# Optimization experiments

Measured on AMD Instinct MI355X. Metric: run time of the kernel, lower is better.

## Reference

```python
import jax, jax.numpy as jnp
import numpy as np

B, T = 128, 512
V, P, K = 10002, 500, 20
DC, DP, DT = 300, 100, 50
D = DC + DP + DT
H = 256


def setup_inputs() -> dict:
    key = jax.random.key(0)
    ks = jax.random.split(key, 21)
    s = lambda i, shape: jax.random.normal(ks[i], shape, jnp.float32) * 0.05
    return dict(
        x=jax.random.randint(ks[0], (B, T), 0, V),
        y=jax.random.randint(ks[1], (B, T), 0, K),
        pre_tags=jax.random.randint(ks[2], (B, T), 0, K),
        pinyin_tags=jax.random.randint(ks[3], (B, T), 0, P),
        mask=jnp.ones((B, T), bool),
        char_emb=s(4, (V, DC)),
        tag_emb=s(5, (K, DT)),
        pinyin_emb=s(6, (P, DP)),
        w_ih_f=s(7, (4 * H, D)), w_hh_f=s(8, (4 * H, H)), b_ih_f=s(9, (4 * H,)), b_hh_f=s(10, (4 * H,)),
        w_ih_b=s(11, (4 * H, D)), w_hh_b=s(12, (4 * H, H)), b_ih_b=s(13, (4 * H,)), b_hh_b=s(14, (4 * H,)),
        w_out=s(15, (K, 2 * H)), b_out=s(16, (K,)),
        start_trans=s(17, (K,)), end_trans=s(18, (K,)), trans=s(19, (K, K)),
    )


def _lstm_dir(xs, w_ih, w_hh, b_ih, b_hh, reverse):
    # xs: [T,B,D]; precompute input projection for all steps (one big GEMM)
    pre = jnp.einsum('tbd,gd->tbg', xs, w_ih) + b_ih + b_hh  # [T,B,4H]
    bsz = xs.shape[1]

    def step(carry, gx):
        h, c = carry
        g = gx + h @ w_hh.T
        i, f, gg, o = jnp.split(g, 4, axis=-1)  # torch gate order i,f,g,o
        c = jax.nn.sigmoid(f) * c + jax.nn.sigmoid(i) * jnp.tanh(gg)
        h = jax.nn.sigmoid(o) * jnp.tanh(c)
        return (h, c), h

    init = (jnp.zeros((bsz, H), xs.dtype), jnp.zeros((bsz, H), xs.dtype))
    _, hs = jax.lax.scan(step, init, pre, reverse=reverse)
    return hs  # [T,B,H]


def _emissions(x, pre_tags, pinyin_tags, char_emb, tag_emb, pinyin_emb,
               w_ih_f, w_hh_f, b_ih_f, b_hh_f, w_ih_b, w_hh_b, b_ih_b, b_hh_b,
               w_out, b_out):
    emb = jnp.concatenate([char_emb[x], pinyin_emb[pinyin_tags], tag_emb[pre_tags]], axis=2)  # [B,T,D]
    xs = emb.transpose(1, 0, 2)  # [T,B,D]
    hf = _lstm_dir(xs, w_ih_f, w_hh_f, b_ih_f, b_hh_f, reverse=False)
    hb = _lstm_dir(xs, w_ih_b, w_hh_b, b_ih_b, b_hh_b, reverse=True)
    h = jnp.concatenate([hf, hb], axis=-1)  # [T,B,2H]
    return jnp.einsum('tbh,kh->tbk', h, w_out) + b_out  # emissions [T,B,K]


def _crf_nll(em, tags, mask, start, trans, end):
    # em [T,B,K] (time-major), torchcrf forward with reduction='sum'
    tg = tags.T  # [T,B]
    mk = mask.T.astype(em.dtype)  # [T,B]
    # gold-path score
    first = start[tg[0]] + jnp.take_along_axis(em[0], tg[0][:, None], 1)[:, 0]

    def num_step(score, inputs):
        e_t, t_prev, t_cur, m = inputs
        s = trans[t_prev, t_cur] + jnp.take_along_axis(e_t, t_cur[:, None], 1)[:, 0]
        return score + s * m, None

    score, _ = jax.lax.scan(num_step, first, (em[1:], tg[:-1], tg[1:], mk[1:]))
    last_idx = (mask.sum(1) - 1).astype(jnp.int32)
    last_tag = jnp.take_along_axis(tags, last_idx[:, None].astype(tags.dtype), 1)[:, 0]
    score = score + end[last_tag]
    # partition function via forward algorithm
    alpha0 = start[None, :] + em[0]  # [B,K]

    def den_step(alpha, inputs):
        e_t, m = inputs
        nxt = jax.nn.logsumexp(alpha[:, :, None] + trans[None, :, :] + e_t[:, None, :], axis=1)
        return jnp.where(m[:, None] > 0, nxt, alpha), None

    alpha, _ = jax.lax.scan(den_step, alpha0, (em[1:], mk[1:]))
    logZ = jax.nn.logsumexp(alpha + end[None, :], axis=1)
    llh = jnp.sum(score - logZ)
    return -llh  # module returns -crf(...)


def reference(x, y, pre_tags, pinyin_tags, mask, char_emb, tag_emb, pinyin_emb,
              w_ih_f, w_hh_f, b_ih_f, b_hh_f, w_ih_b, w_hh_b, b_ih_b, b_hh_b,
              w_out, b_out, start_trans, end_trans, trans):
    em = _emissions(x, pre_tags, pinyin_tags, char_emb, tag_emb, pinyin_emb,
                    w_ih_f, w_hh_f, b_ih_f, b_hh_f, w_ih_b, w_hh_b, b_ih_b, b_hh_b,
                    w_out, b_out)
    return _crf_nll(em, y, mask, start_trans, trans, end_trans)
```

## Files before the change

### kernel.cpp

```cpp
#include <hip/hip_runtime.h>
#include <hip/hip_bf16.h>

typedef __attribute__((ext_vector_type(8))) short short8;
typedef __attribute__((ext_vector_type(4))) float float4v;
typedef __attribute__((ext_vector_type(4))) int int4v;

__device__ __forceinline__ float sigmoidf_(float x) {
  return __fdividef(1.f, 1.f + __expf(-x));
}
__device__ __forceinline__ float tanhf_(float x) {
  float e = __expf(2.f * x);
  return 1.f - __fdividef(2.f, e + 1.f);
}
__device__ __forceinline__ float bflo(unsigned int v) {
  return __uint_as_float(v << 16);
}
__device__ __forceinline__ float bfhi(unsigned int v) {
  return __uint_as_float(v & 0xffff0000u);
}
__device__ __forceinline__ void barrier_lgkm() {
  asm volatile("s_waitcnt lgkmcnt(0)\n\ts_barrier" ::: "memory");
}

__device__ __forceinline__ unsigned int pack4_(float4 v, float inv) {
  int b0 = (int)rintf(v.x * inv), b1 = (int)rintf(v.y * inv);
  int b2 = (int)rintf(v.z * inv), b3 = (int)rintf(v.w * inv);
  return (unsigned int)((b0 & 0xff) | ((b1 & 0xff) << 8) | ((b2 & 0xff) << 16) |
                        ((b3 & 0xff) << 24));
}

__device__ __forceinline__ int sel4_(int4v v, int rr) {
  int a = (rr & 1) ? v[1] : v[0];
  int b = (rr & 1) ? v[3] : v[2];
  return (rr & 2) ? b : a;
}

__global__ __launch_bounds__(256) void wquant_kernel(
    const float* __restrict__ whh_f, const float* __restrict__ whh_b,
    unsigned int* __restrict__ wq, float* __restrict__ wsc) {
  const int wave_g = blockIdx.x * 4 + (threadIdx.x >> 6);
  const int lane = threadIdx.x & 63;
  const int dir = wave_g >> 10, row = wave_g & 1023;
  const float* __restrict__ src = (dir ? whh_b : whh_f) + (size_t)row * 256;
  float4 v = ((const float4*)src)[lane];
  float mx = fmaxf(fmaxf(fabsf(v.x), fabsf(v.y)), fmaxf(fabsf(v.z), fabsf(v.w)));
#pragma unroll
  for (int k = 32; k >= 1; k >>= 1) mx = fmaxf(mx, __shfl_xor(mx, k, 64));
  float inv = (mx > 0.f) ? __fdividef(127.f, mx) : 0.f;
  wq[(size_t)wave_g * 64 + lane] = pack4_(v, inv);
  if (lane == 0) wsc[wave_g] = (mx > 0.f) ? (mx / (127.f * 127.f)) : 0.f;
}

__global__ __launch_bounds__(256) void proj_gemm(
    const float* __restrict__ A, int rowsA, int Kdim, int col_off,
    const float* __restrict__ wf, const float* __restrict__ wb,
    const float* __restrict__ bf1, const float* __restrict__ bf2,
    const float* __restrict__ bb1, const float* __restrict__ bb2,
    __hip_bfloat16* __restrict__ out, int add_bias) {
  __shared__ __align__(16) __hip_bfloat16 As[128][40];
  __shared__ __align__(16) __hip_bfloat16 Bs[256][40];
  const int tid = threadIdx.x;
  const int m0 = blockIdx.x * 128, n0 = blockIdx.y * 256;
  const int lane = tid & 63, wave = tid >> 6;
  const int quad = lane >> 4, lm = lane & 15;
  float4v acc[2][16] = {};
  const int ksteps = (Kdim + 31) >> 5;
  const int r2 = tid >> 1, cbase = (tid & 1) << 4;
  const int rb = tid >> 4, cb = (tid & 15) * 2;
  for (int ks = 0; ks < ksteps; ++ks) {
    const int k0 = ks << 5;
#pragma unroll
    for (int e2 = 0; e2 < 8; ++e2) {
      int kk = k0 + cbase + 2 * e2;
      float b0 = 0.f, b1 = 0.f;
      if (m0 + r2 < rowsA && kk < Kdim) {
        float2 v = *(const float2*)(A + (size_t)(m0 + r2) * Kdim + kk);
        b0 = v.x;
        b1 = v.y;
      }
      As[r2][cbase + 2 * e2] = __float2bfloat16(b0);
      As[r2][cbase + 2 * e2 + 1] = __float2bfloat16(b1);
    }
#pragma unroll
    for (int j = 0; j < 16; ++j) {
      int n = n0 + rb + 16 * j;
      const float* __restrict__ wrow =
          (n < 1024) ? (wf + n * 450 + col_off) : (wb + (n - 1024) * 450 + col_off);
      int kk = k0 + cb;
      float b0 = 0.f, b1 = 0.f;
      if (kk < Kdim) {
        float2 v = *(const float2*)(wrow + kk);
        b0 = v.x;
        b1 = v.y;
      }
      Bs[rb + 16 * j][cb] = __float2bfloat16(b0);
      Bs[rb + 16 * j][cb + 1] = __float2bfloat16(b1);
    }
    __syncthreads();
    short8 af0 = *(const short8*)(&As[wave * 32 + lm][quad * 8]);
    short8 af1 = *(const short8*)(&As[wave * 32 + 16 + lm][quad * 8]);
#pragma unroll
    for (int t = 0; t < 16; ++t) {
      short8 bf = *(const short8*)(&Bs[t * 16 + lm][quad * 8]);
      acc[0][t] = __builtin_amdgcn_mfma_f32_16x16x32_bf16(af0, bf, acc[0][t], 0, 0, 0);
      acc[1][t] = __builtin_amdgcn_mfma_f32_16x16x32_bf16(af1, bf, acc[1][t], 0, 0, 0);
    }
    __syncthreads();
  }
#pragma unroll
  for (int mg = 0; mg < 2; ++mg) {
#pragma unroll
    for (int t = 0; t < 16; ++t) {
#pragma unroll
      for (int rr = 0; rr < 4; ++rr) {
        int m = m0 + wave * 32 + mg * 16 + quad * 4 + rr;
        int col = n0 + t * 16 + lm;
        if (m < rowsA) {
          float v = acc[mg][t][rr];
          if (add_bias)
            v += (col < 1024) ? (bf1[col] + bf2[col]) : (bb1[col - 1024] + bb2[col - 1024]);
          int dir = col >> 10, rq = col & 1023;
          int gate = rq >> 8, u = rq & 255;
          out[m * 2048 + dir * 1024 + u * 4 + gate] = __float2bfloat16(v);
        }
      }
    }
  }
}

__global__ __launch_bounds__(256) void pgsum_kernel(
    const __hip_bfloat16* __restrict__ pin, const __hip_bfloat16* __restrict__ tag,
    __hip_bfloat16* __restrict__ pg) {
  const int r = blockIdx.x;
  const int p = r / 20, g = r - p * 20;
  const int i = threadIdx.x;
  const short8 va = *(const short8*)(pin + (size_t)p * 2048 + i * 8);
  const short8 vb = *(const short8*)(tag + (size_t)g * 2048 + i * 8);
  short8 vo;
#pragma unroll
  for (int j = 0; j < 8; ++j) {
    float a = __uint_as_float(((unsigned)(unsigned short)va[j]) << 16);
    float b = __uint_as_float(((unsigned)(unsigned short)vb[j]) << 16);
    __hip_bfloat16 o = __float2bfloat16(a + b);
    vo[j] = *(short*)&o;
  }
  *(short8*)(pg + (size_t)r * 2048 + i * 8) = vo;
}

template <int USE_PG>
__global__ __launch_bounds__(512, 2) void lstm_kernel(
    const unsigned int* __restrict__ wq, const float* __restrict__ wsc,
    const int* __restrict__ x, const int* __restrict__ ptags, const int* __restrict__ gtags,
    const char* __restrict__ char_proj, const char* __restrict__ pin_proj,
    const char* __restrict__ tag_proj, const char* __restrict__ pg_proj,
    __hip_bfloat16* __restrict__ h_out) {
  extern __shared__ __align__(16) char smem[];
  char* hqb = smem;

  const int tid = threadIdx.x;
  const int w = tid >> 6, lane = tid & 63;
  const int quad = lane >> 4, lm = lane & 15;
  const int sel = lm >> 1;
  const int mt = sel >> 2, rr = sel & 3;
  const int unit = w * 32 + mt * 16 + quad * 4 + rr;
  const int chain = blockIdx.x;
  const int dir = chain >> 7;
  const int b = chain & 127;
  const int boff = b * 512;

  if (tid < 34) ((uint4*)hqb)[tid] = make_uint4(0, 0, 0, 0);

  const unsigned int* __restrict__ wqd = wq + (size_t)dir * 65536;
  int4v Wf[4][2][4];
#pragma unroll
  for (int g = 0; g < 4; ++g)
#pragma unroll
    for (int m = 0; m < 2; ++m) {
      const int row = g * 256 + w * 32 + m * 16 + lm;
#pragma unroll
      for (int kt = 0; kt < 4; ++kt)
        Wf[g][m][kt] = *(const int4v*)(wqd + row * 64 + kt * 16 + quad * 4);
    }
  float sc4[4];
#pragma unroll
  for (int g = 0; g < 4; ++g) sc4[g] = wsc[dir * 1024 + g * 256 + unit];
  __syncthreads();

  const int pre_off = dir * 2048 + unit * 8;
  float cst = 0.f;
  int4v kZero = {0, 0, 0, 0};
  asm volatile("" : "+v"(kZero));

  uint2 vc, vp, vg;
  int xn, pgn, pn, gn;
  {
    const int t0 = dir ? 511 : 0;
    int xc = x[boff + t0], pc = ptags[boff + t0], gc = gtags[boff + t0];
    vc = *(const uint2*)(char_proj + (size_t)xc * 4096 + pre_off);
    if (USE_PG) {
      vp = *(const uint2*)(pg_proj + (size_t)(pc * 20 + gc) * 4096 + pre_off);
    } else {
      vp = *(const uint2*)(pin_proj + (size_t)pc * 4096 + pre_off);
      vg = *(const uint2*)(tag_proj + (size_t)gc * 4096 + pre_off);
    }
    const int t1 = dir ? 510 : 1;
    xn = x[boff + t1];
    pn = ptags[boff + t1];
    gn = gtags[boff + t1];
    if (USE_PG) pgn = pn * 20 + gn;
  }

  int4v Bv[4];
#pragma unroll
  for (int kt = 0; kt < 4; ++kt)
    Bv[kt] = *(const int4v*)(hqb + kt * 64 + quad * 16);

  __hip_bfloat16* __restrict__ hrow = h_out + (size_t)chain * 512 * 256 + unit;

  for (int s = 0; s < 512; ++s) {
    const int nxt = (s & 1) ^ 1;
    const uint2 cv = vc, pv = vp, gv = vg;
    vc = *(const uint2*)(char_proj + (size_t)xn * 4096 + pre_off);
    if (USE_PG) {
      vp = *(const uint2*)(pg_proj + (size_t)pgn * 4096 + pre_off);
    } else {
      vp = *(const uint2*)(pin_proj + (size_t)pn * 4096 + pre_off);
      vg = *(const uint2*)(tag_proj + (size_t)gn * 4096 + pre_off);
    }
    {
      const int k2 = (s + 2 < 512) ? s + 2 : 511;
      const int t2 = dir ? 511 - k2 : k2;
      xn = x[boff + t2];
      pn = ptags[boff + t2];
      gn = gtags[boff + t2];
      if (USE_PG) pgn = pn * 20 + gn;
    }

    int4v acc[4][2];
#pragma unroll
    for (int g = 0; g < 4; ++g)
#pragma unroll
      for (int m = 0; m < 2; ++m)
        acc[g][m] = __builtin_amdgcn_mfma_i32_16x16x64_i8(Wf[g][m][0], Bv[0], kZero, 0, 0, 0);
#pragma unroll
    for (int kt = 1; kt < 4; ++kt) {
#pragma unroll
      for (int g = 0; g < 4; ++g)
#pragma unroll
        for (int m = 0; m < 2; ++m)
          acc[g][m] = __builtin_amdgcn_mfma_i32_16x16x64_i8(Wf[g][m][kt], Bv[kt], acc[g][m], 0, 0, 0);
    }

    int ai = mt ? sel4_(acc[0][1], rr) : sel4_(acc[0][0], rr);
    int af = mt ? sel4_(acc[1][1], rr) : sel4_(acc[1][0], rr);
    int ag = mt ? sel4_(acc[2][1], rr) : sel4_(acc[2][0], rr);
    int ao = mt ? sel4_(acc[3][1], rr) : sel4_(acc[3][0], rr);
    float gi, gf, gg, go;
    if (USE_PG) {
      gi = bflo(cv.x) + bflo(pv.x) + (float)ai * sc4[0];
      gf = bfhi(cv.x) + bfhi(pv.x) + (float)af * sc4[1];
      gg = bflo(cv.y) + bflo(pv.y) + (float)ag * sc4[2];
      go = bfhi(cv.y) + bfhi(pv.y) + (float)ao * sc4[3];
    } else {
      gi = bflo(cv.x) + bflo(pv.x) + bflo(gv.x) + (float)ai * sc4[0];
      gf = bfhi(cv.x) + bfhi(pv.x) + bfhi(gv.x) + (float)af * sc4[1];
      gg = bflo(cv.y) + bflo(pv.y) + bflo(gv.y) + (float)ag * sc4[2];
      go = bfhi(cv.y) + bfhi(pv.y) + bfhi(gv.y) + (float)ao * sc4[3];
    }
    cst = sigmoidf_(gf) * cst + sigmoidf_(gi) * tanhf_(gg);
    float hval = sigmoidf_(go) * tanhf_(cst);
    if (!(lm & 1)) {
      ((signed char*)hqb)[nxt * 272 + unit] = (signed char)(int)rintf(hval * 127.f);
    }
    barrier_lgkm();
#pragma unroll
    for (int kt = 0; kt < 4; ++kt)
      Bv[kt] = *(const int4v*)(hqb + nxt * 272 + kt * 64 + quad * 16);
    if (!(lm & 1)) {
      const int tcur = dir ? 511 - s : s;
      hrow[(size_t)tcur * 256] = __float2bfloat16(hval);
    }
  }
}

__global__ __launch_bounds__(256) void emis_kernel(
    const __hip_bfloat16* __restrict__ h_glob, const float* __restrict__ w_out,
    const float* __restrict__ b_out, float* __restrict__ em) {
  __shared__ __align__(16) __hip_bfloat16 As[64][40];
  __shared__ __align__(16) __hip_bfloat16 Bs[32][40];
  const int tid = threadIdx.x;
  const int n0 = blockIdx.x * 64;
  const int lane = tid & 63, wave = tid >> 6, quad = lane >> 4, lm = lane & 15;
  float4v acc[2] = {};
  const int r = tid >> 2, c0 = (tid & 3) << 3;
  const int rb = tid >> 3, cb = (tid & 7) << 2;
  for (int ks = 0; ks < 16; ++ks) {
    const int j0 = ks * 32;
    const int dirk = j0 >> 8, jin = j0 & 255;
    const int n = n0 + r, bb = n >> 9, tt = n & 511;
    const uint4* src =
        (const uint4*)(h_glob + ((size_t)(dirk * 128 + bb) * 512 + tt) * 256 + jin + c0);
    *(uint4*)(&As[r][c0]) = *src;
#pragma unroll
    for (int e = 0; e < 4; ++e) {
      float v = (rb < 20) ? w_out[rb * 512 + j0 + cb + e] : 0.f;
      Bs[rb][cb + e] = __float2bfloat16(v);
    }
    __syncthreads();
    short8 af = *(const short8*)(&As[wave * 16 + lm][quad * 8]);
#pragma unroll
    for (int t2 = 0; t2 < 2; ++t2) {
      short8 bf = *(const short8*)(&Bs[t2 * 16 + lm][quad * 8]);
      acc[t2] = __builtin_amdgcn_mfma_f32_16x16x32_bf16(af, bf, acc[t2], 0, 0, 0);
    }
    __syncthreads();
  }
#pragma unroll
  for (int t2 = 0; t2 < 2; ++t2) {
#pragma unroll
    for (int rr = 0; rr < 4; ++rr) {
      int col = t2 * 16 + lm;
      if (col < 20) {
        int n = n0 + wave * 16 + quad * 4 + rr;
        em[(size_t)n * 20 + col] = acc[t2][rr] + b_out[col];
      }
    }
  }
}

__global__ __launch_bounds__(64) void crf_kernel(
    const float* __restrict__ em, const int* __restrict__ y,
    const float* __restrict__ start_trans, const float* __restrict__ end_trans,
    const float* __restrict__ trans, float* __restrict__ partials) {
  const int b = blockIdx.x;
  const int lane = threadIdx.x;
  const int jj = lane < 20 ? lane : 19;
  const bool act = lane < 20;
  const float* __restrict__ emb = em + (size_t)b * 512 * 20;
  const int* __restrict__ yb = y + b * 512;

  float s_part = 0.f;
#pragma unroll
  for (int i = 0; i < 8; ++i) {
    int t = lane + 64 * i;
    int yc = yb[t];
    float v = emb[t * 20 + yc];
    v += (t == 0) ? start_trans[yc] : trans[yb[t - 1] * 20 + yc];
    s_part += v;
  }
#pragma unroll
  for (int k = 32; k >= 1; k >>= 1) s_part += __shfl_xor(s_part, k, 64);
  float score = s_part + end_trans[yb[511]];

  float ET[20];
#pragma unroll
  for (int i = 0; i < 20; ++i) ET[i] = __expf(trans[i * 20 + jj]);
  float alpha = act ? (start_trans[jj] + emb[jj]) : -1e30f;
  float P = alpha;
#pragma unroll
  for (int k = 32; k >= 1; k >>= 1) P = fmaxf(P, __shfl_xor(P, k, 64));

  float eC = emb[1 * 20 + jj];
  float eN = emb[2 * 20 + jj];
  for (int t = 1; t < 512; ++t) {
    if ((t & 15) == 0) {
      P = alpha;
#pragma unroll
      for (int k = 32; k >= 1; k >>= 1) P = fmaxf(P, __shfl_xor(P, k, 64));
    }
    float ex = __expf(alpha - P);
    float s0 = 0.f, s1 = 0.f;
#pragma unroll
    for (int i = 0; i < 20; i += 2) {
      float e0 = __int_as_float(__builtin_amdgcn_readlane(__float_as_int(ex), i));
      float e1 = __int_as_float(__builtin_amdgcn_readlane(__float_as_int(ex), i + 1));
      s0 = fmaf(e0, ET[i], s0);
      s1 = fmaf(e1, ET[i + 1], s1);
    }
    int tf = t + 2 < 512 ? t + 2 : 511;
    float eF = emb[tf * 20 + jj];
    if (act) alpha = P + __logf(s0 + s1) + eC;
    eC = eN;
    eN = eF;
  }
  float v = act ? (alpha + end_trans[jj]) : -1e30f;
  float Pz = v;
#pragma unroll
  for (int k = 32; k >= 1; k >>= 1) Pz = fmaxf(Pz, __shfl_xor(Pz, k, 64));
  float e2 = __expf(v - Pz);
#pragma unroll
  for (int k = 32; k >= 1; k >>= 1) e2 += __shfl_xor(e2, k, 64);
  float logZ = Pz + __logf(e2);
  if (lane == 0) partials[b] = logZ - score;
}

__global__ __launch_bounds__(128) void reduce_kernel(const float* __restrict__ partials,
                                                     float* __restrict__ out) {
  const int tid = threadIdx.x;
  float v = partials[tid];
#pragma unroll
  for (int k = 32; k >= 1; k >>= 1) v += __shfl_xor(v, k, 64);
  __shared__ float tmp[2];
  if ((tid & 63) == 0) tmp[tid >> 6] = v;
  __syncthreads();
  if (tid == 0) out[0] = tmp[0] + tmp[1];
}

extern "C" void kernel_launch(void* const* d_in, const int* in_sizes, int n_in,
                              void* d_out, int out_size, void* d_ws, size_t ws_size,
                              hipStream_t stream) {
  const int* x = (const int*)d_in[0];
  const int* y = (const int*)d_in[1];
  const int* pre_tags = (const int*)d_in[2];
  const int* pinyin_tags = (const int*)d_in[3];
  const float* char_emb = (const float*)d_in[5];
  const float* tag_emb = (const float*)d_in[6];
  const float* pinyin_emb = (const float*)d_in[7];
  const float* w_ih_f = (const float*)d_in[8];
  const float* w_hh_f = (const float*)d_in[9];
  const float* b_ih_f = (const float*)d_in[10];
  const float* b_hh_f = (const float*)d_in[11];
  const float* w_ih_b = (const float*)d_in[12];
  const float* w_hh_b = (const float*)d_in[13];
  const float* b_ih_b = (const float*)d_in[14];
  const float* b_hh_b = (const float*)d_in[15];
  const float* w_out = (const float*)d_in[16];
  const float* b_out = (const float*)d_in[17];
  const float* start_trans = (const float*)d_in[18];
  const float* end_trans = (const float*)d_in[19];
  const float* trans = (const float*)d_in[20];

  char* ws = (char*)d_ws;
  __hip_bfloat16* char_proj = (__hip_bfloat16*)(ws);
  __hip_bfloat16* pin_proj = (__hip_bfloat16*)(ws + 40968192);
  __hip_bfloat16* tag_proj = (__hip_bfloat16*)(ws + 43016192);
  __hip_bfloat16* h_glob = (__hip_bfloat16*)(ws + 43098112);
  float* em = (float*)(ws + 110206976);
  float* partials = (float*)(ws + 115449856);
  unsigned int* wq = (unsigned int*)(ws + 110206976);
  float* wsc = (float*)(ws + 110206976 + 524288);
  __hip_bfloat16* pg_proj = (__hip_bfloat16*)(ws + 115450368);
  const bool use_pg = ws_size >= (size_t)115450368 + 40960000;

  wquant_kernel<<<512, 256, 0, stream>>>(w_hh_f, w_hh_b, wq, wsc);

  proj_gemm<<<dim3(79, 8), 256, 0, stream>>>(char_emb, 10002, 300, 0, w_ih_f, w_ih_b,
                                             nullptr, nullptr, nullptr, nullptr, char_proj, 0);
  proj_gemm<<<dim3(4, 8), 256, 0, stream>>>(pinyin_emb, 500, 100, 300, w_ih_f, w_ih_b,
                                            nullptr, nullptr, nullptr, nullptr, pin_proj, 0);
  proj_gemm<<<dim3(1, 8), 256, 0, stream>>>(tag_emb, 20, 50, 400, w_ih_f, w_ih_b,
                                            b_ih_f, b_hh_f, b_ih_b, b_hh_b, tag_proj, 1);
  if (use_pg) pgsum_kernel<<<10000, 256, 0, stream>>>(pin_proj, tag_proj, pg_proj);

  const int lstm_lds = 1024;
  if (use_pg) {
    hipFuncSetAttribute((const void*)lstm_kernel<1>, hipFuncAttributeMaxDynamicSharedMemorySize,
                        lstm_lds);
    lstm_kernel<1><<<256, 512, lstm_lds, stream>>>(wq, wsc, x, pinyin_tags, pre_tags,
                                                   (const char*)char_proj, (const char*)pin_proj,
                                                   (const char*)tag_proj, (const char*)pg_proj,
                                                   h_glob);
  } else {
    hipFuncSetAttribute((const void*)lstm_kernel<0>, hipFuncAttributeMaxDynamicSharedMemorySize,
                        lstm_lds);
    lstm_kernel<0><<<256, 512, lstm_lds, stream>>>(wq, wsc, x, pinyin_tags, pre_tags,
                                                   (const char*)char_proj, (const char*)pin_proj,
                                                   (const char*)tag_proj, (const char*)pg_proj,
                                                   h_glob);
  }

  emis_kernel<<<1024, 256, 0, stream>>>(h_glob, w_out, b_out, em);
  crf_kernel<<<128, 64, 0, stream>>>(em, y, start_trans, end_trans, trans, partials);
  reduce_kernel<<<1, 128, 0, stream>>>(partials, (float*)d_out);
}
```

Measured before the change: 947.0 us.

## Fuse emission GEMM into CRF kernel with emissions kept in LDS

Merges the emission projection and the CRF forward pass into one kernel with one block per batch row. Each block converts w_out to bf16 in LDS, computes all 512x20 emissions with MFMA, and keeps them in LDS. The CRF recurrence then reads from LDS instead of global memory. The kernel launch and the global em round-trip go away, but the GEMM now runs on only 128 blocks instead of 1024, so it uses less parallelism. The recurrence's inner dot product is also split into four accumulators.

```diff
diff --git a/kernel.cpp b/kernel.cpp
--- a/kernel.cpp
+++ b/kernel.cpp
@@ -283,60 +283,70 @@
   }
 }
 
-__global__ __launch_bounds__(256) void emis_kernel(
+__global__ __launch_bounds__(256) void emcrf_kernel(
     const __hip_bfloat16* __restrict__ h_glob, const float* __restrict__ w_out,
-    const float* __restrict__ b_out, float* __restrict__ em) {
-  __shared__ __align__(16) __hip_bfloat16 As[64][40];
-  __shared__ __align__(16) __hip_bfloat16 Bs[32][40];
+    const float* __restrict__ b_out, const int* __restrict__ y,
+    const float* __restrict__ start_trans, const float* __restrict__ end_trans,
+    const float* __restrict__ trans, float* __restrict__ partials) {
+  extern __shared__ __align__(16) char smem2[];
+  float* emL = (float*)smem2;
+  __hip_bfloat16* wL = (__hip_bfloat16*)(smem2 + 40960);
+
+  const int b = blockIdx.x;
   const int tid = threadIdx.x;
-  const int n0 = blockIdx.x * 64;
-  const int lane = tid & 63, wave = tid >> 6, quad = lane >> 4, lm = lane & 15;
-  float4v acc[2] = {};
-  const int r = tid >> 2, c0 = (tid & 3) << 3;
-  const int rb = tid >> 3, cb = (tid & 7) << 2;
+  const int wave = tid >> 6, lane = tid & 63;
+  const int quad = lane >> 4, lm = lane & 15;
+
+  for (int i = tid; i < 10240; i += 256) {
+    const int r = i >> 9, c = i & 511;
+    wL[r * 520 + c] = __float2bfloat16(w_out[i]);
+  }
+  __syncthreads();
+
+  float bo[2];
+#pragma unroll
+  for (int t2 = 0; t2 < 2; ++t2) {
+    const int col = t2 * 16 + lm;
+    bo[t2] = (col < 20) ? b_out[col] : 0.f;
+  }
+  const int col0ok = lm < 16;
+  const int col1ok = (16 + lm) < 20;
+  float4v acc[8][2] = {};
+  const int trow = wave * 16 + lm;
   for (int ks = 0; ks < 16; ++ks) {
     const int j0 = ks * 32;
     const int dirk = j0 >> 8, jin = j0 & 255;
-    const int n = n0 + r, bb = n >> 9, tt = n & 511;
-    const uint4* src =
-        (const uint4*)(h_glob + ((size_t)(dirk * 128 + bb) * 512 + tt) * 256 + jin + c0);
-    *(uint4*)(&As[r][c0]) = *src;
-#pragma unroll
-    for (int e = 0; e < 4; ++e) {
-      float v = (rb < 20) ? w_out[rb * 512 + j0 + cb + e] : 0.f;
-      Bs[rb][cb + e] = __float2bfloat16(v);
-    }
-    __syncthreads();
-    short8 af = *(const short8*)(&As[wave * 16 + lm][quad * 8]);
+    short8 bf0 = {}, bf1 = {};
+    if (col0ok) bf0 = *(const short8*)(wL + lm * 520 + j0 + quad * 8);
+    if (col1ok) bf1 = *(const short8*)(wL + (16 + lm) * 520 + j0 + quad * 8);
+    const __hip_bfloat16* __restrict__ hbase =
+        h_glob + ((size_t)(dirk * 128 + b) * 512 + trow) * 256 + jin + quad * 8;
+#pragma unroll
+    for (int st = 0; st < 8; ++st) {
+      short8 af = *(const short8*)(hbase + (size_t)st * 64 * 256);
+      acc[st][0] = __builtin_amdgcn_mfma_f32_16x16x32_bf16(af, bf0, acc[st][0], 0, 0, 0);
+      acc[st][1] = __builtin_amdgcn_mfma_f32_16x16x32_bf16(af, bf1, acc[st][1], 0, 0, 0);
+    }
+  }
+#pragma unroll
+  for (int st = 0; st < 8; ++st) {
 #pragma unroll
     for (int t2 = 0; t2 < 2; ++t2) {
-      short8 bf = *(const short8*)(&Bs[t2 * 16 + lm][quad * 8]);
-      acc[t2] = __builtin_amdgcn_mfma_f32_16x16x32_bf16(af, bf, acc[t2], 0, 0, 0);
-    }
-    __syncthreads();
-  }
-#pragma unroll
-  for (int t2 = 0; t2 < 2; ++t2) {
-#pragma unroll
-    for (int rr = 0; rr < 4; ++rr) {
-      int col = t2 * 16 + lm;
+      const int col = t2 * 16 + lm;
       if (col < 20) {
-        int n = n0 + wave * 16 + quad * 4 + rr;
-        em[(size_t)n * 20 + col] = acc[t2][rr] + b_out[col];
+#pragma unroll
+        for (int rr = 0; rr < 4; ++rr) {
+          const int n = st * 64 + wave * 16 + quad * 4 + rr;
+          emL[n * 20 + col] = acc[st][t2][rr] + bo[t2];
+        }
       }
     }
   }
-}
-
-__global__ __launch_bounds__(64) void crf_kernel(
-    const float* __restrict__ em, const int* __restrict__ y,
-    const float* __restrict__ start_trans, const float* __restrict__ end_trans,
-    const float* __restrict__ trans, float* __restrict__ partials) {
-  const int b = blockIdx.x;
-  const int lane = threadIdx.x;
+  __syncthreads();
+  if (wave != 0) return;
+
   const int jj = lane < 20 ? lane : 19;
   const bool act = lane < 20;
-  const float* __restrict__ emb = em + (size_t)b * 512 * 20;
   const int* __restrict__ yb = y + b * 512;
 
   float s_part = 0.f;
@@ -344,7 +354,7 @@
   for (int i = 0; i < 8; ++i) {
     int t = lane + 64 * i;
     int yc = yb[t];
-    float v = emb[t * 20 + yc];
+    float v = emL[t * 20 + yc];
     v += (t == 0) ? start_trans[yc] : trans[yb[t - 1] * 20 + yc];
     s_part += v;
   }
@@ -355,42 +365,41 @@
   float ET[20];
 #pragma unroll
   for (int i = 0; i < 20; ++i) ET[i] = __expf(trans[i * 20 + jj]);
-  float alpha = act ? (start_trans[jj] + emb[jj]) : -1e30f;
+  float alpha = act ? (start_trans[jj] + emL[jj]) : -1e30f;
   float P = alpha;
 #pragma unroll
   for (int k = 32; k >= 1; k >>= 1) P = fmaxf(P, __shfl_xor(P, k, 64));
 
-  float eC = emb[1 * 20 + jj];
-  float eN = emb[2 * 20 + jj];
   for (int t = 1; t < 512; ++t) {
+    float eCur = emL[t * 20 + jj];
     if ((t & 15) == 0) {
       P = alpha;
 #pragma unroll
       for (int k = 32; k >= 1; k >>= 1) P = fmaxf(P, __shfl_xor(P, k, 64));
     }
     float ex = __expf(alpha - P);
-    float s0 = 0.f, s1 = 0.f;
-#pragma unroll
-    for (int i = 0; i < 20; i += 2) {
+    float s0 = 0.f, s1 = 0.f, s2 = 0.f, s3 = 0.f;
+#pragma unroll
+    for (int i = 0; i < 20; i += 4) {
       float e0 = __int_as_float(__builtin_amdgcn_readlane(__float_as_int(ex), i));
       float e1 = __int_as_float(__builtin_amdgcn_readlane(__float_as_int(ex), i + 1));
+      float e2 = __int_as_float(__builtin_amdgcn_readlane(__float_as_int(ex), i + 2));
+      float e3 = __int_as_float(__builtin_amdgcn_readlane(__float_as_int(ex), i + 3));
       s0 = fmaf(e0, ET[i], s0);
       s1 = fmaf(e1, ET[i + 1], s1);
-    }
-    int tf = t + 2 < 512 ? t + 2 : 511;
-    float eF = emb[tf * 20 + jj];
-    if (act) alpha = P + __logf(s0 + s1) + eC;
-    eC = eN;
-    eN = eF;
+      s2 = fmaf(e2, ET[i + 2], s2);
+      s3 = fmaf(e3, ET[i + 3], s3);
+    }
+    if (act) alpha = P + __logf((s0 + s1) + (s2 + s3)) + eCur;
   }
   float v = act ? (alpha + end_trans[jj]) : -1e30f;
   float Pz = v;
 #pragma unroll
   for (int k = 32; k >= 1; k >>= 1) Pz = fmaxf(Pz, __shfl_xor(Pz, k, 64));
-  float e2 = __expf(v - Pz);
-#pragma unroll
-  for (int k = 32; k >= 1; k >>= 1) e2 += __shfl_xor(e2, k, 64);
-  float logZ = Pz + __logf(e2);
+  float e2s = __expf(v - Pz);
+#pragma unroll
+  for (int k = 32; k >= 1; k >>= 1) e2s += __shfl_xor(e2s, k, 64);
+  float logZ = Pz + __logf(e2s);
   if (lane == 0) partials[b] = logZ - score;
 }
 
@@ -435,7 +444,6 @@
   __hip_bfloat16* pin_proj = (__hip_bfloat16*)(ws + 40968192);
   __hip_bfloat16* tag_proj = (__hip_bfloat16*)(ws + 43016192);
   __hip_bfloat16* h_glob = (__hip_bfloat16*)(ws + 43098112);
-  float* em = (float*)(ws + 110206976);
   float* partials = (float*)(ws + 115449856);
   unsigned int* wq = (unsigned int*)(ws + 110206976);
   float* wsc = (float*)(ws + 110206976 + 524288);
@@ -469,7 +477,10 @@
                                                    h_glob);
   }
 
-  emis_kernel<<<1024, 256, 0, stream>>>(h_glob, w_out, b_out, em);
-  crf_kernel<<<128, 64, 0, stream>>>(em, y, start_trans, end_trans, trans, partials);
+  const int emcrf_lds = 61760;
+  hipFuncSetAttribute((const void*)emcrf_kernel, hipFuncAttributeMaxDynamicSharedMemorySize,
+                      emcrf_lds);
+  emcrf_kernel<<<128, 256, emcrf_lds, stream>>>(h_glob, w_out, b_out, y, start_trans,
+                                                end_trans, trans, partials);
   reduce_kernel<<<1, 128, 0, stream>>>(partials, (float*)d_out);
 }
```

After: 938.4 us. Within noise of the previous version (-0.9%).
